# Optimization experiments

Hardware: AMD Instinct MI355X
Metric: run time of the kernel (lower is better)

The kernel has to match this reference:

```python
import jax, jax.numpy as jnp
import numpy as np

B, S, Nv, D, DF, H = 8, 1024, 768, 512, 2048, 8
DH = D // H
EPS = 1e-5


def _layernorm(x, g, b):
    mu = jnp.mean(x, axis=-1, keepdims=True)
    var = jnp.mean((x - mu) ** 2, axis=-1, keepdims=True)
    return (x - mu) * jax.lax.rsqrt(var + EPS) * g + b


def _mha(x, Wq, Wk, Wv, Wo):
    b, s, d = x.shape
    q = (x @ Wq).reshape(b, s, H, DH)
    k = (x @ Wk).reshape(b, s, H, DH)
    v = (x @ Wv).reshape(b, s, H, DH)
    scores = jnp.einsum('bqhd,bkhd->bhqk', q, k) / np.sqrt(DH).astype(np.float32)
    a = jax.nn.softmax(scores, axis=-1)
    o = jnp.einsum('bhqk,bkhd->bqhd', a, v).reshape(b, s, d)
    return o @ Wo


def setup_inputs() -> dict:
    key = jax.random.key(0)
    ks = jax.random.split(key, 20)
    sc = 1.0 / np.sqrt(D)
    scf = 1.0 / np.sqrt(DF)
    n = lambda k, shp, s: (jax.random.normal(k, shp, jnp.float32) * s)
    return {
        'x': n(ks[0], (B, S, D), 1.0),
        'idx_emb_1': jax.random.randint(ks[1], (B, Nv), 0, Nv, dtype=jnp.int64) if jax.config.jax_enable_x64 else jax.random.randint(ks[1], (B, Nv), 0, Nv).astype(jnp.int32),
        'idx_pro_1': jax.random.randint(ks[2], (B, Nv), 0, Nv).astype(jnp.int32),
        'N': Nv,
        'Wq1': n(ks[3], (D, D), sc), 'Wk1': n(ks[4], (D, D), sc),
        'Wv1': n(ks[5], (D, D), sc), 'Wo1': n(ks[6], (D, D), sc),
        'Wq2': n(ks[7], (D, D), sc), 'Wk2': n(ks[8], (D, D), sc),
        'Wv2': n(ks[9], (D, D), sc), 'Wo2': n(ks[10], (D, D), sc),
        'w_conv1': n(ks[11], (D, DF), sc), 'b_conv1': jnp.zeros((DF,), jnp.float32),
        'w_conv2': n(ks[12], (DF, D), scf), 'b_conv2': jnp.zeros((D,), jnp.float32),
        'g1': jnp.ones((D,), jnp.float32), 'beta1': jnp.zeros((D,), jnp.float32),
        'g2': jnp.ones((D,), jnp.float32), 'beta2': jnp.zeros((D,), jnp.float32),
    }


def reference(x, idx_emb_1, idx_pro_1, N,
              Wq1, Wk1, Wv1, Wo1, Wq2, Wk2, Wv2, Wo2,
              w_conv1, b_conv1, w_conv2, b_conv2, g1, beta1, g2, beta2):
    # batched gather-reorder of first N tokens; rest pass through
    x_l1 = x.at[:, :N].set(jnp.take_along_axis(x[:, :N], idx_emb_1[:, :, None].astype(jnp.int32), axis=1))
    attn1 = _mha(x_l1, Wq1, Wk1, Wv1, Wo1)
    attn2 = jnp.flip(_mha(jnp.flip(x_l1, axis=1), Wq2, Wk2, Wv2, Wo2), axis=1)
    new_x1 = attn1 + attn2
    x_l2 = new_x1.at[:, :N].set(jnp.take_along_axis(new_x1[:, :N], idx_pro_1[:, :, None].astype(jnp.int32), axis=1))
    x = _layernorm(x + x_l2, g1, beta1)
    # kernel-size-1 Conv1d FFN == pointwise linear (dropout=0, eval mode)
    y = jnp.maximum(x @ w_conv1 + b_conv1, 0.0)
    y = y @ w_conv2 + b_conv2
    out = _layernorm(x + y, g2, beta2)
    return (out, attn1, attn2)
```

## Files before the change

### kernel.cpp

```cpp
#include <hip/hip_runtime.h>
#include <hip/hip_bf16.h>
#include <stdint.h>

#define B_ 8
#define S_ 1024
#define NV_ 768
#define D_ 512
#define DF_ 2048
#define H_ 8
#define DH_ 64
#define BS_ (B_*S_)
#define BSD_ ((size_t)B_*S_*D_)
#define QKVLD 3072

typedef __bf16 bf16x8 __attribute__((ext_vector_type(8)));
typedef float f32x4 __attribute__((ext_vector_type(4)));
typedef float f32x16 __attribute__((ext_vector_type(16)));
typedef __hip_bfloat16 bf16;

__device__ __forceinline__ void async_copy16(const void* g, void* l) {
  __builtin_amdgcn_global_load_lds((const __attribute__((address_space(1))) void*)g,
                                   (__attribute__((address_space(3))) void*)l, 16, 0, 0);
}

__device__ __forceinline__ void stage_tile(const bf16* __restrict__ g, int gRow0, long ldg,
                                           int gCol0, bf16* lds, int rows, int tid) {
  const int totalBytes = rows << 7;
  for (int off = tid * 16; off < totalBytes; off += 4096) {
    const int r = off >> 7;
    const int c = off & 127;
    const int srcByte = c ^ ((r & 7) << 4);
    const bf16* gp = g + (long)(gRow0 + r) * ldg + gCol0 + (srcByte >> 1);
    async_copy16(gp, (char*)lds + off);
  }
}

__device__ __forceinline__ bf16x8 lds_frag(const bf16* base, int row, int kElem) {
  const int byte = (row << 7) + ((kElem << 1) ^ ((row & 7) << 4));
  return *(const bf16x8*)((const char*)base + byte);
}

template<int BASE>
__device__ __forceinline__ bf16x8 p_frag(const f32x16& s) {
  union { ushort u[8]; bf16x8 b; } r;
#pragma unroll
  for (int e = 0; e < 8; e++)
    r.u[e] = __bfloat16_as_ushort(__float2bfloat16(s[BASE + e]));
  return r.b;
}

__device__ __forceinline__ bf16x8 ones_frag() {
  union { ushort u[8]; bf16x8 b; } r;
#pragma unroll
  for (int e = 0; e < 8; e++) r.u[e] = 0x3F80;
  return r.b;
}

__device__ __forceinline__ f32x16 zero16() {
  f32x16 z;
#pragma unroll
  for (int i = 0; i < 16; i++) z[i] = 0.f;
  return z;
}

struct WP8 { const float* p[8]; };
__global__ __launch_bounds__(256) void wtrans8_kernel(WP8 ws, bf16* __restrict__ dstBase) {
  __shared__ float tile[32][33];
  const int z = blockIdx.z;
  const float sc = (z == 0 || z == 3) ? 0.1803368801f : 1.f;
  const float* __restrict__ src = ws.p[z];
  bf16* __restrict__ dst = dstBase + (size_t)z * D_ * D_;
  const int tx = threadIdx.x, ty = threadIdx.y;
  const int n0 = blockIdx.x * 32, k0 = blockIdx.y * 32;
#pragma unroll
  for (int i = 0; i < 4; i++) tile[ty + i * 8][tx] = src[(long)(k0 + ty + i * 8) * D_ + n0 + tx];
  __syncthreads();
#pragma unroll
  for (int i = 0; i < 4; i++)
    dst[(long)(n0 + ty + i * 8) * D_ + k0 + tx] = __float2bfloat16(tile[tx][ty + i * 8] * sc);
}

__global__ __launch_bounds__(256) void wtrans_kernel(const float* __restrict__ src,
                                                     bf16* __restrict__ dst, int K, int N) {
  __shared__ float tile[32][33];
  const int tx = threadIdx.x, ty = threadIdx.y;
  const int n0 = blockIdx.x * 32, k0 = blockIdx.y * 32;
#pragma unroll
  for (int i = 0; i < 4; i++) tile[ty + i * 8][tx] = src[(long)(k0 + ty + i * 8) * N + n0 + tx];
  __syncthreads();
#pragma unroll
  for (int i = 0; i < 4; i++)
    dst[(long)(n0 + ty + i * 8) * K + k0 + tx] = __float2bfloat16(tile[tx][ty + i * 8]);
}

__global__ __launch_bounds__(256) void vtrans_kernel(const bf16* __restrict__ qkv,
                                                     bf16* __restrict__ vtb) {
  __shared__ bf16 tile[32][33];
  const int tx = threadIdx.x, ty = threadIdx.y;
  const int s0 = blockIdx.x * 32, d0 = blockIdx.y * 32;
  const int z = blockIdx.z;
  const int set = z >> 6, bh = z & 63;
  const bf16* sp = qkv + (long)(bh >> 3) * S_ * QKVLD + set * 1536 + 1024 + (bh & 7) * 64;
  bf16* dp = vtb + (long)z * DH_ * S_;
#pragma unroll
  for (int i = 0; i < 4; i++) tile[ty + i * 8][tx] = sp[(long)(s0 + ty + i * 8) * QKVLD + d0 + tx];
  __syncthreads();
  const int c = s0 + tx;
  const int cp = (c & ~12) | ((c & 4) << 1) | ((c & 8) >> 1);
#pragma unroll
  for (int i = 0; i < 4; i++) dp[(long)(d0 + ty + i * 8) * S_ + cp] = tile[tx][ty + i * 8];
}

__global__ __launch_bounds__(256) void gather_cvt_kernel(const float* __restrict__ x,
                                                         const int* __restrict__ idx,
                                                         const int* __restrict__ Np,
                                                         bf16* __restrict__ out) {
  const int N = *Np;
  const int row = blockIdx.x * 2 + (threadIdx.x >> 7);
  const int t = threadIdx.x & 127;
  const int b = row >> 10, s = row & 1023;
  const int src = (s < N) ? idx[b * NV_ + s] : s;
  const float4 v = *(const float4*)(x + ((long)b * S_ + src) * D_ + t * 4);
  ushort4 u;
  u.x = (ushort)__bfloat16_as_ushort(__float2bfloat16(v.x));
  u.y = (ushort)__bfloat16_as_ushort(__float2bfloat16(v.y));
  u.z = (ushort)__bfloat16_as_ushort(__float2bfloat16(v.z));
  u.w = (ushort)__bfloat16_as_ushort(__float2bfloat16(v.w));
  *(ushort4*)(out + (long)row * D_ + t * 4) = u;
}

template<int BM, int BN, int MR, int NR, int OUTF, int BIAS, int RELU>
__global__ __launch_bounds__(256) void gemm_bt(const bf16* __restrict__ A, long lda, long sAz,
                                               const bf16* __restrict__ Bt, long sBz,
                                               const float* __restrict__ bias,
                                               void* __restrict__ C, long ldc, long sCz,
                                               int K) {
  constexpr int WC = BN / (NR * 16);
  constexpr int WR = BM / (MR * 16);
  static_assert(WR * WC == 4, "4 waves");
  __shared__ bf16 As[BM * 64];
  __shared__ bf16 Bs[BN * 64];
  const int tid = threadIdx.x;
  const int lane = tid & 63, wave = tid >> 6;
  const int wr = wave / WC, wc = wave % WC;
  const int g = lane >> 4, lr = lane & 15;
  const int m0 = blockIdx.x * BM, n0 = blockIdx.y * BN;
  const int z = blockIdx.z;
  A += (long)z * sAz;
  Bt += (long)z * sBz;

  f32x4 acc[MR][NR];
#pragma unroll
  for (int m = 0; m < MR; m++)
#pragma unroll
    for (int n = 0; n < NR; n++) acc[m][n] = (f32x4){0.f, 0.f, 0.f, 0.f};

  for (int kt = 0; kt < K; kt += 64) {
    stage_tile(A, m0, lda, kt, As, BM, tid);
    stage_tile(Bt, n0, K, kt, Bs, BN, tid);
    __syncthreads();
#pragma unroll
    for (int ks = 0; ks < 64; ks += 32) {
      const int kk = ks + g * 8;
      bf16x8 aF[MR], bF[NR];
#pragma unroll
      for (int m = 0; m < MR; m++) aF[m] = lds_frag(As, wr * (MR * 16) + m * 16 + lr, kk);
#pragma unroll
      for (int n = 0; n < NR; n++) bF[n] = lds_frag(Bs, wc * (NR * 16) + n * 16 + lr, kk);
#pragma unroll
      for (int m = 0; m < MR; m++)
#pragma unroll
        for (int n = 0; n < NR; n++)
          acc[m][n] = __builtin_amdgcn_mfma_f32_16x16x32_bf16(aF[m], bF[n], acc[m][n], 0, 0, 0);
    }
    __syncthreads();
  }

#pragma unroll
  for (int m = 0; m < MR; m++) {
#pragma unroll
    for (int n = 0; n < NR; n++) {
      const int row = m0 + wr * (MR * 16) + m * 16 + g * 4;
      const int col = n0 + wc * (NR * 16) + n * 16 + lr;
      const float bv = BIAS ? bias[col] : 0.f;
#pragma unroll
      for (int r = 0; r < 4; r++) {
        float v = acc[m][n][r] + bv;
        if (RELU) v = fmaxf(v, 0.f);
        if (OUTF) ((float*)C)[(long)z * sCz + (long)(row + r) * ldc + col] = v;
        else ((bf16*)C)[(long)z * sCz + (long)(row + r) * ldc + col] = __float2bfloat16(v);
      }
    }
  }
}

__global__ __launch_bounds__(256, 4) void flash_kernel(bf16* __restrict__ qkv,
                                                       const bf16* __restrict__ vtb) {
  __shared__ char lds[32768];
  const int tid = threadIdx.x;
  const int lane = tid & 63, warp = tid >> 6;
  const int qlo = lane & 31, hi = lane >> 5;

  const int bid = (int)blockIdx.x;
  const int swz = (bid & 7) * 128 + (bid >> 3);
  const int qt = swz & 7;
  const int sbh = swz >> 3;
  const int set = sbh >> 6;
  const int b = (sbh >> 3) & 7, h = sbh & 7;

  bf16* Qp = qkv + (long)b * S_ * QKVLD + set * 1536 + h * DH_;
  const bf16* Kp = Qp + 512;
  const bf16* Vp = vtb + (long)sbh * DH_ * S_;

  bf16* const buf0 = (bf16*)(lds + 16384);
  bf16* const buf1 = (bf16*)lds;

  stage_tile(Qp, qt * 128, QKVLD, 0, (bf16*)lds, 128, tid);
  stage_tile(Kp, 0, QKVLD, 0, buf0, 64, tid);
  stage_tile(Vp, 0, S_, 0, buf0 + 4096, 64, tid);
  __syncthreads();

  bf16x8 qFh[4];
#pragma unroll
  for (int d4 = 0; d4 < 4; d4++)
    qFh[d4] = lds_frag((bf16*)lds, warp * 32 + qlo, d4 * 16 + hi * 8);
  __syncthreads();

  stage_tile(Kp, 64, QKVLD, 0, buf1, 64, tid);
  stage_tile(Vp, 0, S_, 64, buf1 + 4096, 64, tid);

  f32x16 oAcc0 = zero16(), oAcc1 = zero16(), sAcc = zero16();
  float mrun = -INFINITY;
  const bf16x8 onesF = ones_frag();

  for (int t = 0; t < 16; t++) {
    bf16* const Kb = (t & 1) ? buf1 : buf0;
    bf16* const Vb = Kb + 4096;

    f32x16 s0 = zero16(), s1 = zero16();
    __builtin_amdgcn_s_setprio(1);
#pragma unroll
    for (int d4 = 0; d4 < 4; d4++) {
      const int kc = d4 * 16 + hi * 8;
      s0 = __builtin_amdgcn_mfma_f32_32x32x16_bf16(lds_frag(Kb, qlo, kc), qFh[d4], s0, 0, 0, 0);
      s1 = __builtin_amdgcn_mfma_f32_32x32x16_bf16(lds_frag(Kb, 32 + qlo, kc), qFh[d4], s1, 0, 0, 0);
    }
    __builtin_amdgcn_s_setprio(0);

    float mx = fmaxf(s0[0], s0[1]);
#pragma unroll
    for (int r = 2; r < 16; r++) mx = fmaxf(mx, s0[r]);
#pragma unroll
    for (int r = 0; r < 16; r++) mx = fmaxf(mx, s1[r]);
    mx = fmaxf(mx, __shfl_xor(mx, 32, 64));

    if (!__all(mx - mrun <= 11.5f)) {
      const float mnew = fmaxf(mrun, mx);
      const float resc = exp2f(mrun - mnew);
      mrun = mnew;
#pragma unroll
      for (int r = 0; r < 16; r++) {
        const float rs = __shfl(resc, (r & 3) + 8 * (r >> 2) + 4 * hi, 64);
        oAcc0[r] *= rs;
        oAcc1[r] *= rs;
        sAcc[r] *= rs;
      }
    }

#pragma unroll
    for (int r = 0; r < 16; r++) s0[r] = exp2f(s0[r] - mrun);
#pragma unroll
    for (int r = 0; r < 16; r++) s1[r] = exp2f(s1[r] - mrun);

    __builtin_amdgcn_s_setprio(1);
    {
      const bf16x8 pa0 = p_frag<0>(s0);
      oAcc0 = __builtin_amdgcn_mfma_f32_32x32x16_bf16(pa0, lds_frag(Vb, qlo, hi * 8), oAcc0, 0, 0, 0);
      oAcc1 = __builtin_amdgcn_mfma_f32_32x32x16_bf16(pa0, lds_frag(Vb, 32 + qlo, hi * 8), oAcc1, 0, 0, 0);
      sAcc = __builtin_amdgcn_mfma_f32_32x32x16_bf16(pa0, onesF, sAcc, 0, 0, 0);
      const bf16x8 pa1 = p_frag<8>(s0);
      oAcc0 = __builtin_amdgcn_mfma_f32_32x32x16_bf16(pa1, lds_frag(Vb, qlo, 16 + hi * 8), oAcc0, 0, 0, 0);
      oAcc1 = __builtin_amdgcn_mfma_f32_32x32x16_bf16(pa1, lds_frag(Vb, 32 + qlo, 16 + hi * 8), oAcc1, 0, 0, 0);
      sAcc = __builtin_amdgcn_mfma_f32_32x32x16_bf16(pa1, onesF, sAcc, 0, 0, 0);
      const bf16x8 pa2 = p_frag<0>(s1);
      oAcc0 = __builtin_amdgcn_mfma_f32_32x32x16_bf16(pa2, lds_frag(Vb, qlo, 32 + hi * 8), oAcc0, 0, 0, 0);
      oAcc1 = __builtin_amdgcn_mfma_f32_32x32x16_bf16(pa2, lds_frag(Vb, 32 + qlo, 32 + hi * 8), oAcc1, 0, 0, 0);
      sAcc = __builtin_amdgcn_mfma_f32_32x32x16_bf16(pa2, onesF, sAcc, 0, 0, 0);
      const bf16x8 pa3 = p_frag<8>(s1);
      oAcc0 = __builtin_amdgcn_mfma_f32_32x32x16_bf16(pa3, lds_frag(Vb, qlo, 48 + hi * 8), oAcc0, 0, 0, 0);
      oAcc1 = __builtin_amdgcn_mfma_f32_32x32x16_bf16(pa3, lds_frag(Vb, 32 + qlo, 48 + hi * 8), oAcc1, 0, 0, 0);
      sAcc = __builtin_amdgcn_mfma_f32_32x32x16_bf16(pa3, onesF, sAcc, 0, 0, 0);
    }
    __builtin_amdgcn_s_setprio(0);

    __syncthreads();
    if (t + 2 < 16) {
      stage_tile(Kp, (t + 2) * 64, QKVLD, 0, Kb, 64, tid);
      stage_tile(Vp, 0, S_, (t + 2) * 64, Kb + 4096, 64, tid);
    }
  }

#pragma unroll
  for (int r = 0; r < 16; r++) {
    const int q = (r & 3) + 8 * (r >> 2) + 4 * hi;
    const float linv = 1.f / sAcc[r];
    bf16* op = Qp + (long)(qt * 128 + warp * 32 + q) * QKVLD;
    op[qlo] = __float2bfloat16(oAcc0[r] * linv);
    op[32 + qlo] = __float2bfloat16(oAcc1[r] * linv);
  }
}

__global__ __launch_bounds__(256) void fuse1_kernel(const float* __restrict__ x,
                                                    const float* __restrict__ a1,
                                                    const float* __restrict__ a2,
                                                    const int* __restrict__ idx,
                                                    const int* __restrict__ Np,
                                                    const float* __restrict__ gw,
                                                    const float* __restrict__ bw,
                                                    bf16* __restrict__ xlnB) {
  const int N = *Np;
  const int row = blockIdx.x * 4 + (threadIdx.x >> 6);
  const int lane = threadIdx.x & 63;
  const int b = row >> 10, s = row & 1023;
  const int j = (s < N) ? idx[b * NV_ + s] : s;
  const float* xp = x + (long)row * D_ + lane * 8;
  const float* p1 = a1 + ((long)b * S_ + j) * D_ + lane * 8;
  const float* p2 = a2 + ((long)b * S_ + j) * D_ + lane * 8;
  float v[8];
  float sum = 0.f;
#pragma unroll
  for (int q = 0; q < 2; q++) {
    const float4 t = ((const float4*)xp)[q];
    const float4 u = ((const float4*)p1)[q];
    const float4 w = ((const float4*)p2)[q];
    v[q * 4 + 0] = t.x + u.x + w.x; v[q * 4 + 1] = t.y + u.y + w.y;
    v[q * 4 + 2] = t.z + u.z + w.z; v[q * 4 + 3] = t.w + u.w + w.w;
  }
#pragma unroll
  for (int i = 0; i < 8; i++) sum += v[i];
#pragma unroll
  for (int o = 1; o < 64; o <<= 1) sum += __shfl_xor(sum, o, 64);
  const float mu = sum * (1.f / D_);
  float var = 0.f;
#pragma unroll
  for (int i = 0; i < 8; i++) { const float t = v[i] - mu; var += t * t; }
#pragma unroll
  for (int o = 1; o < 64; o <<= 1) var += __shfl_xor(var, o, 64);
  const float rs = rsqrtf(var * (1.f / D_) + 1e-5f);
#pragma unroll
  for (int i = 0; i < 8; i++) {
    const int d = lane * 8 + i;
    xlnB[(long)row * D_ + d] = __float2bfloat16((v[i] - mu) * rs * gw[d] + bw[d]);
  }
}

__global__ __launch_bounds__(256) void fuse2_kernel(const bf16* __restrict__ xlnB,
                                                    const bf16* __restrict__ ybf,
                                                    const float* __restrict__ gw,
                                                    const float* __restrict__ bw,
                                                    float* __restrict__ out) {
  const int row = blockIdx.x * 4 + (threadIdx.x >> 6);
  const int lane = threadIdx.x & 63;
  const bf16* xp = xlnB + (long)row * D_ + lane * 8;
  const bf16* yp = ybf + (long)row * D_ + lane * 8;
  float v[8];
  float sum = 0.f;
#pragma unroll
  for (int i = 0; i < 8; i++) {
    v[i] = __bfloat162float(xp[i]) + __bfloat162float(yp[i]);
    sum += v[i];
  }
#pragma unroll
  for (int o = 1; o < 64; o <<= 1) sum += __shfl_xor(sum, o, 64);
  const float mu = sum * (1.f / D_);
  float var = 0.f;
#pragma unroll
  for (int i = 0; i < 8; i++) { const float t = v[i] - mu; var += t * t; }
#pragma unroll
  for (int o = 1; o < 64; o <<= 1) var += __shfl_xor(var, o, 64);
  const float rs = rsqrtf(var * (1.f / D_) + 1e-5f);
#pragma unroll
  for (int i = 0; i < 8; i++) {
    const int d = lane * 8 + i;
    out[(long)row * D_ + d] = (v[i] - mu) * rs * gw[d] + bw[d];
  }
}

extern "C" void kernel_launch(void* const* d_in, const int* in_sizes, int n_in,
                              void* d_out, int out_size, void* d_ws, size_t ws_size,
                              hipStream_t stream) {
  const float* x   = (const float*)d_in[0];
  const int* idx1  = (const int*)d_in[1];
  const int* idx2  = (const int*)d_in[2];
  const int* Np    = (const int*)d_in[3];
  const float* b_conv1 = (const float*)d_in[13];
  const float* b_conv2 = (const float*)d_in[15];
  const float* g1    = (const float*)d_in[16];
  const float* beta1 = (const float*)d_in[17];
  const float* g2    = (const float*)d_in[18];
  const float* beta2 = (const float*)d_in[19];

  float* outp  = (float*)d_out;
  float* attn1 = outp + BSD_;

  const size_t DD = (size_t)D_ * D_;
  char* w = (char*)d_ws;
  bf16* wT  = (bf16*)w;
  bf16* w1T = wT + 8 * DD;
  bf16* w2T = w1T + (size_t)DF_ * D_;
  bf16* qkv = (bf16*)(w + (8ll << 20));
  bf16* xl1 = (bf16*)(w + (56ll << 20));
  bf16* vtb = (bf16*)(w + (56ll << 20));
  bf16* xlnB = (bf16*)(w + (56ll << 20));
  bf16* ffn = (bf16*)(w + (8ll << 20));
  bf16* ybf = (bf16*)(w + (40ll << 20));

  WP8 wp;
  wp.p[0] = (const float*)d_in[4];
  wp.p[1] = (const float*)d_in[5];
  wp.p[2] = (const float*)d_in[6];
  wp.p[3] = (const float*)d_in[8];
  wp.p[4] = (const float*)d_in[9];
  wp.p[5] = (const float*)d_in[10];
  wp.p[6] = (const float*)d_in[7];
  wp.p[7] = (const float*)d_in[11];

  const dim3 tb(32, 8);
  wtrans8_kernel<<<dim3(16, 16, 8), tb, 0, stream>>>(wp, wT);
  wtrans_kernel<<<dim3(DF_ / 32, D_ / 32), tb, 0, stream>>>((const float*)d_in[12], w1T, D_, DF_);
  wtrans_kernel<<<dim3(D_ / 32, DF_ / 32), tb, 0, stream>>>((const float*)d_in[14], w2T, DF_, D_);

  gather_cvt_kernel<<<BS_ / 2, 256, 0, stream>>>(x, idx1, Np, xl1);

  gemm_bt<128, 128, 4, 4, 0, 0, 0><<<dim3(BS_ / 128, QKVLD / 128, 1), 256, 0, stream>>>(
      xl1, D_, 0, wT, 0, nullptr, qkv, QKVLD, 0, D_);

  vtrans_kernel<<<dim3(S_ / 32, DH_ / 32, 128), tb, 0, stream>>>(qkv, vtb);

  flash_kernel<<<1024, 256, 0, stream>>>(qkv, vtb);

  gemm_bt<128, 64, 4, 2, 1, 0, 0><<<dim3(BS_ / 128, D_ / 64, 2), 256, 0, stream>>>(
      qkv, QKVLD, 1536, wT + 6 * DD, (long)DD, nullptr, attn1, D_, (long)BSD_, D_);

  fuse1_kernel<<<BS_ / 4, 256, 0, stream>>>(x, attn1, attn1 + BSD_, idx2, Np, g1, beta1, xlnB);

  gemm_bt<128, 128, 4, 4, 0, 1, 1><<<dim3(BS_ / 128, DF_ / 128, 1), 256, 0, stream>>>(
      xlnB, D_, 0, w1T, 0, b_conv1, ffn, DF_, 0, D_);
  gemm_bt<128, 64, 4, 2, 0, 1, 0><<<dim3(BS_ / 128, D_ / 64, 1), 256, 0, stream>>>(
      ffn, DF_, 0, w2T, 0, b_conv2, ybf, D_, 0, DF_);

  fuse2_kernel<<<BS_ / 4, 256, 0, stream>>>(xlnB, ybf, g2, beta2, outp);
}
```

Baseline: 218.4 us.

## Replace softmax exp2 with bit-trick exponent and retune LDS swizzle in attention

In the flash-attention kernel, the per-element exp2f and bf16 conversion are replaced by a Schraudolph-style integer trick: fmaf(s, 2^23, bias) cast to int yields float bits, and the upper halves are packed into bf16 pairs with v_perm. A new XOR swizzle pattern (fswz) is used for LDS staging and fragment reads of Q/K/V, aimed at reducing bank conflicts. The max reduction uses three-input fmax and the rescale uses the hardware exp2 builtin. The approximate exponent loses accuracy relative to exp2f, which may affect numerical tolerance.

```diff
diff --git a/kernel.cpp b/kernel.cpp
--- a/kernel.cpp
+++ b/kernel.cpp
@@ -34,18 +34,43 @@
     async_copy16(gp, (char*)lds + off);
   }
 }
-
 __device__ __forceinline__ bf16x8 lds_frag(const bf16* base, int row, int kElem) {
   const int byte = (row << 7) + ((kElem << 1) ^ ((row & 7) << 4));
   return *(const bf16x8*)((const char*)base + byte);
 }
 
+__device__ __forceinline__ int fswz(int row) {
+  return ((((row >> 3) & 3) << 1) | (row & 1)) << 4;
+}
+__device__ __forceinline__ void stage_tile_f(const bf16* __restrict__ g, int gRow0, long ldg,
+                                             int gCol0, bf16* lds, int rows, int tid) {
+  const int totalBytes = rows << 7;
+  for (int off = tid * 16; off < totalBytes; off += 4096) {
+    const int r = off >> 7;
+    const int c = off & 127;
+    const int srcByte = c ^ fswz(r);
+    const bf16* gp = g + (long)(gRow0 + r) * ldg + gCol0 + (srcByte >> 1);
+    async_copy16(gp, (char*)lds + off);
+  }
+}
+__device__ __forceinline__ bf16x8 lds_frag_f(const bf16* base, int row, int kElem) {
+  const int byte = (row << 7) + ((kElem << 1) ^ fswz(row));
+  return *(const bf16x8*)((const char*)base + byte);
+}
+
+__device__ __forceinline__ float fmax3_(float a, float b, float c) {
+  return fmaxf(fmaxf(a, b), c);
+}
+
 template<int BASE>
-__device__ __forceinline__ bf16x8 p_frag(const f32x16& s) {
-  union { ushort u[8]; bf16x8 b; } r;
-#pragma unroll
-  for (int e = 0; e < 8; e++)
-    r.u[e] = __bfloat16_as_ushort(__float2bfloat16(s[BASE + e]));
+__device__ __forceinline__ bf16x8 pexp_frag(const f32x16& s, float mb) {
+  union { unsigned u[4]; bf16x8 b; } r;
+#pragma unroll
+  for (int e = 0; e < 4; e++) {
+    const int i0 = (int)fmaf(s[BASE + 2 * e], 8388608.f, mb);
+    const int i1 = (int)fmaf(s[BASE + 2 * e + 1], 8388608.f, mb);
+    r.u[e] = __builtin_amdgcn_perm((unsigned)i1, (unsigned)i0, 0x07060302u);
+  }
   return r.b;
 }
 
@@ -215,19 +240,19 @@
   bf16* const buf0 = (bf16*)(lds + 16384);
   bf16* const buf1 = (bf16*)lds;
 
-  stage_tile(Qp, qt * 128, QKVLD, 0, (bf16*)lds, 128, tid);
-  stage_tile(Kp, 0, QKVLD, 0, buf0, 64, tid);
-  stage_tile(Vp, 0, S_, 0, buf0 + 4096, 64, tid);
+  stage_tile_f(Qp, qt * 128, QKVLD, 0, (bf16*)lds, 128, tid);
+  stage_tile_f(Kp, 0, QKVLD, 0, buf0, 64, tid);
+  stage_tile_f(Vp, 0, S_, 0, buf0 + 4096, 64, tid);
   __syncthreads();
 
   bf16x8 qFh[4];
 #pragma unroll
   for (int d4 = 0; d4 < 4; d4++)
-    qFh[d4] = lds_frag((bf16*)lds, warp * 32 + qlo, d4 * 16 + hi * 8);
+    qFh[d4] = lds_frag_f((bf16*)lds, warp * 32 + qlo, d4 * 16 + hi * 8);
   __syncthreads();
 
-  stage_tile(Kp, 64, QKVLD, 0, buf1, 64, tid);
-  stage_tile(Vp, 0, S_, 64, buf1 + 4096, 64, tid);
+  stage_tile_f(Kp, 64, QKVLD, 0, buf1, 64, tid);
+  stage_tile_f(Vp, 0, S_, 64, buf1 + 4096, 64, tid);
 
   f32x16 oAcc0 = zero16(), oAcc1 = zero16(), sAcc = zero16();
   float mrun = -INFINITY;
@@ -242,21 +267,21 @@
 #pragma unroll
     for (int d4 = 0; d4 < 4; d4++) {
       const int kc = d4 * 16 + hi * 8;
-      s0 = __builtin_amdgcn_mfma_f32_32x32x16_bf16(lds_frag(Kb, qlo, kc), qFh[d4], s0, 0, 0, 0);
-      s1 = __builtin_amdgcn_mfma_f32_32x32x16_bf16(lds_frag(Kb, 32 + qlo, kc), qFh[d4], s1, 0, 0, 0);
+      s0 = __builtin_amdgcn_mfma_f32_32x32x16_bf16(lds_frag_f(Kb, qlo, kc), qFh[d4], s0, 0, 0, 0);
+      s1 = __builtin_amdgcn_mfma_f32_32x32x16_bf16(lds_frag_f(Kb, 32 + qlo, kc), qFh[d4], s1, 0, 0, 0);
     }
     __builtin_amdgcn_s_setprio(0);
 
     float mx = fmaxf(s0[0], s0[1]);
 #pragma unroll
-    for (int r = 2; r < 16; r++) mx = fmaxf(mx, s0[r]);
-#pragma unroll
-    for (int r = 0; r < 16; r++) mx = fmaxf(mx, s1[r]);
+    for (int r = 2; r < 16; r += 2) mx = fmax3_(mx, s0[r], s0[r + 1]);
+#pragma unroll
+    for (int r = 0; r < 16; r += 2) mx = fmax3_(mx, s1[r], s1[r + 1]);
     mx = fmaxf(mx, __shfl_xor(mx, 32, 64));
 
     if (!__all(mx - mrun <= 11.5f)) {
       const float mnew = fmaxf(mrun, mx);
-      const float resc = exp2f(mrun - mnew);
+      const float resc = __builtin_amdgcn_exp2f(mrun - mnew);
       mrun = mnew;
 #pragma unroll
       for (int r = 0; r < 16; r++) {
@@ -267,36 +292,33 @@
       }
     }
 
-#pragma unroll
-    for (int r = 0; r < 16; r++) s0[r] = exp2f(s0[r] - mrun);
-#pragma unroll
-    for (int r = 0; r < 16; r++) s1[r] = exp2f(s1[r] - mrun);
+    const float mb = 1064872540.f - mrun * 8388608.f;
 
     __builtin_amdgcn_s_setprio(1);
     {
-      const bf16x8 pa0 = p_frag<0>(s0);
-      oAcc0 = __builtin_amdgcn_mfma_f32_32x32x16_bf16(pa0, lds_frag(Vb, qlo, hi * 8), oAcc0, 0, 0, 0);
-      oAcc1 = __builtin_amdgcn_mfma_f32_32x32x16_bf16(pa0, lds_frag(Vb, 32 + qlo, hi * 8), oAcc1, 0, 0, 0);
+      const bf16x8 pa0 = pexp_frag<0>(s0, mb);
+      oAcc0 = __builtin_amdgcn_mfma_f32_32x32x16_bf16(pa0, lds_frag_f(Vb, qlo, hi * 8), oAcc0, 0, 0, 0);
+      oAcc1 = __builtin_amdgcn_mfma_f32_32x32x16_bf16(pa0, lds_frag_f(Vb, 32 + qlo, hi * 8), oAcc1, 0, 0, 0);
       sAcc = __builtin_amdgcn_mfma_f32_32x32x16_bf16(pa0, onesF, sAcc, 0, 0, 0);
-      const bf16x8 pa1 = p_frag<8>(s0);
-      oAcc0 = __builtin_amdgcn_mfma_f32_32x32x16_bf16(pa1, lds_frag(Vb, qlo, 16 + hi * 8), oAcc0, 0, 0, 0);
-      oAcc1 = __builtin_amdgcn_mfma_f32_32x32x16_bf16(pa1, lds_frag(Vb, 32 + qlo, 16 + hi * 8), oAcc1, 0, 0, 0);
+      const bf16x8 pa1 = pexp_frag<8>(s0, mb);
+      oAcc0 = __builtin_amdgcn_mfma_f32_32x32x16_bf16(pa1, lds_frag_f(Vb, qlo, 16 + hi * 8), oAcc0, 0, 0, 0);
+      oAcc1 = __builtin_amdgcn_mfma_f32_32x32x16_bf16(pa1, lds_frag_f(Vb, 32 + qlo, 16 + hi * 8), oAcc1, 0, 0, 0);
       sAcc = __builtin_amdgcn_mfma_f32_32x32x16_bf16(pa1, onesF, sAcc, 0, 0, 0);
-      const bf16x8 pa2 = p_frag<0>(s1);
-      oAcc0 = __builtin_amdgcn_mfma_f32_32x32x16_bf16(pa2, lds_frag(Vb, qlo, 32 + hi * 8), oAcc0, 0, 0, 0);
-      oAcc1 = __builtin_amdgcn_mfma_f32_32x32x16_bf16(pa2, lds_frag(Vb, 32 + qlo, 32 + hi * 8), oAcc1, 0, 0, 0);
+      const bf16x8 pa2 = pexp_frag<0>(s1, mb);
+      oAcc0 = __builtin_amdgcn_mfma_f32_32x32x16_bf16(pa2, lds_frag_f(Vb, qlo, 32 + hi * 8), oAcc0, 0, 0, 0);
+      oAcc1 = __builtin_amdgcn_mfma_f32_32x32x16_bf16(pa2, lds_frag_f(Vb, 32 + qlo, 32 + hi * 8), oAcc1, 0, 0, 0);
       sAcc = __builtin_amdgcn_mfma_f32_32x32x16_bf16(pa2, onesF, sAcc, 0, 0, 0);
-      const bf16x8 pa3 = p_frag<8>(s1);
-      oAcc0 = __builtin_amdgcn_mfma_f32_32x32x16_bf16(pa3, lds_frag(Vb, qlo, 48 + hi * 8), oAcc0, 0, 0, 0);
-      oAcc1 = __builtin_amdgcn_mfma_f32_32x32x16_bf16(pa3, lds_frag(Vb, 32 + qlo, 48 + hi * 8), oAcc1, 0, 0, 0);
+      const bf16x8 pa3 = pexp_frag<8>(s1, mb);
+      oAcc0 = __builtin_amdgcn_mfma_f32_32x32x16_bf16(pa3, lds_frag_f(Vb, qlo, 48 + hi * 8), oAcc0, 0, 0, 0);
+      oAcc1 = __builtin_amdgcn_mfma_f32_32x32x16_bf16(pa3, lds_frag_f(Vb, 32 + qlo, 48 + hi * 8), oAcc1, 0, 0, 0);
       sAcc = __builtin_amdgcn_mfma_f32_32x32x16_bf16(pa3, onesF, sAcc, 0, 0, 0);
     }
     __builtin_amdgcn_s_setprio(0);
 
     __syncthreads();
     if (t + 2 < 16) {
-      stage_tile(Kp, (t + 2) * 64, QKVLD, 0, Kb, 64, tid);
-      stage_tile(Vp, 0, S_, (t + 2) * 64, Kb + 4096, 64, tid);
+      stage_tile_f(Kp, (t + 2) * 64, QKVLD, 0, Kb, 64, tid);
+      stage_tile_f(Vp, 0, S_, (t + 2) * 64, Kb + 4096, 64, tid);
     }
   }
 
```

Result: faster. 204.7 us (-6.3%).
